# Performance work log

Measured on AMD Instinct MI355X. Metric: run time of the kernel, lower is better.

Reference implementation:

```python
import jax, jax.numpy as jnp
import numpy as np

B, N, D, R, STEPS = 16, 512, 512, 8, 2


def setup_inputs() -> dict:
    key = jax.random.key(0)
    ks = jax.random.split(key, 8)
    nodes = jax.random.normal(ks[0], (B, N, D), dtype=jnp.float32)
    edges = jax.random.uniform(ks[1], (B, R, N, N), dtype=jnp.float32)
    scale = 1.0 / np.sqrt(D)
    # per-relation Linear layers: weight [out,in] torch-style, bias [out]
    msg_W = jax.random.uniform(ks[2], (R, D, D), minval=-scale, maxval=scale, dtype=jnp.float32)
    msg_b = jax.random.uniform(ks[3], (R, D), minval=-scale, maxval=scale, dtype=jnp.float32)
    # GRUCell params, gate order (r, z, n) like torch
    w_ih = jax.random.uniform(ks[4], (3 * D, D), minval=-scale, maxval=scale, dtype=jnp.float32)
    w_hh = jax.random.uniform(ks[5], (3 * D, D), minval=-scale, maxval=scale, dtype=jnp.float32)
    b_ih = jax.random.uniform(ks[6], (3 * D,), minval=-scale, maxval=scale, dtype=jnp.float32)
    b_hh = jax.random.uniform(ks[7], (3 * D,), minval=-scale, maxval=scale, dtype=jnp.float32)
    return {"nodes": nodes, "edges": edges, "msg_W": msg_W, "msg_b": msg_b,
            "w_ih": w_ih, "w_hh": w_hh, "b_ih": b_ih, "b_hh": b_hh}


def reference(nodes, edges, msg_W, msg_b, w_ih, w_hh, b_ih, b_hh):
    # nodes: [b,n,d], edges: [b,R,n,n]
    h = nodes  # keep [b,n,d]; torch flattens to [b*n,d] but math is identical
    bias_sum = msg_b.sum(axis=0)  # sum of per-relation biases, [d]
    for _ in range(STEPS):
        # per-relation message passing: m[b,r,i,d] = edges[b,r] @ h[b]
        m = jnp.einsum('brij,bjd->brid', edges, h)
        # per-relation Linear (y = x @ W_r^T + b_r), summed over relations
        agg = jnp.einsum('brid,red->bie', m, msg_W) + bias_sum  # [b,n,d]
        # GRUCell update (gate order r, z, n)
        gi = agg @ w_ih.T + b_ih  # [b,n,3d]
        gh = h @ w_hh.T + b_hh    # [b,n,3d]
        ir, iz, i_n = jnp.split(gi, 3, axis=-1)
        hr, hz, h_n = jnp.split(gh, 3, axis=-1)
        r = jax.nn.sigmoid(ir + hr)
        z = jax.nn.sigmoid(iz + hz)
        n_t = jnp.tanh(i_n + r * h_n)
        h = (1.0 - z) * n_t + z * h
    return h.mean(axis=1)  # [b,d]
```

## Files before the change

kernel.cpp:

```cpp
#include <hip/hip_runtime.h>

typedef _Float16 f16;
typedef __attribute__((ext_vector_type(8))) _Float16 half8;
typedef __attribute__((ext_vector_type(4))) float f32x4;

struct f16x4 { f16 a, b, c, d; };


__global__ void cvt_fr(const float* __restrict__ in, f16* __restrict__ hi,
                       f16* __restrict__ lo, int n_units) {
  const int u = blockIdx.x * blockDim.x + threadIdx.x;
  if (u >= n_units) return;
  const int l = u & 63, kc = (u >> 6) & 15, rt = u >> 10;
  const long ibase = (long)(rt * 16 + (l & 15)) * 512 + kc * 32 + ((l >> 4) << 3);
  const float4 v0 = *(const float4*)(in + ibase);
  const float4 v1 = *(const float4*)(in + ibase + 4);
  const float v[8] = {v0.x, v0.y, v0.z, v0.w, v1.x, v1.y, v1.z, v1.w};
  half8 h, lw;
#pragma unroll
  for (int e = 0; e < 8; ++e) {
    h[e] = (f16)v[e];
    lw[e] = (f16)(v[e] - (float)h[e]);
  }
  *(half8*)(hi + (long)u * 8) = h;
  *(half8*)(lo + (long)u * 8) = lw;
}

__global__ void cvt_fr1(const float* __restrict__ in, f16* __restrict__ hi,
                        int n_units) {
  const int u = blockIdx.x * blockDim.x + threadIdx.x;
  if (u >= n_units) return;
  const int l = u & 63, kc = (u >> 6) & 15, rt = u >> 10;
  const long ibase = (long)(rt * 16 + (l & 15)) * 512 + kc * 32 + ((l >> 4) << 3);
  const float4 v0 = *(const float4*)(in + ibase);
  const float4 v1 = *(const float4*)(in + ibase + 4);
  const float v[8] = {v0.x, v0.y, v0.z, v0.w, v1.x, v1.y, v1.z, v1.w};
  half8 h;
#pragma unroll
  for (int e = 0; e < 8; ++e) h[e] = (f16)v[e];
  *(half8*)(hi + (long)u * 8) = h;
}

__global__ void bias_sum_k(const float* __restrict__ msg_b, float* __restrict__ bs) {
  int e = threadIdx.x;
  float s = 0.f;
  for (int r = 0; r < 8; ++r) s += msg_b[r * 512 + e];
  bs[e] = s;
}

template <int SA, int SB, int OUT, int SWZ>
__global__ __launch_bounds__(256, 2) void gemm_dr(
    const f16* __restrict__ Ah, const f16* __restrict__ Al,
    const f16* __restrict__ Bh, const f16* __restrict__ Bl,
    f16* __restrict__ Chi, f16* __restrict__ Clo, float* __restrict__ Cf,
    const float* __restrict__ bias, int N, int R, long sAr, long sBr,
    int zdiv, long sAzr, long sAzb, long sBzr, long sBzb,
    long sCzr, long sCzb) {
  __shared__ __align__(16) f16 smem[16384];
  const int tid = threadIdx.x;
  int bx, by, z;
  if constexpr (SWZ) {
    const int l = blockIdx.x;
    const int xcd = l & 7, m2 = l >> 3, zq = m2 >> 4, t = m2 & 15;
    z = (zq << 3) | xcd; bx = t & 3; by = t >> 2;
  } else {
    bx = blockIdx.x; by = blockIdx.y; z = blockIdx.z;
  }
  const int zr = z % zdiv, zb = z / zdiv;
  const int lane = tid & 63;
  const int w = tid >> 6;
  const int wm = (w & 1) << 6;
  const int wn = (w >> 1) << 6;

  const f16* pAh = Ah + (long)zr * sAzr + (long)zb * sAzb +
                   (long)(by * 8 + (wm >> 4)) * 8192 + lane * 8;
  const f16* pBh = Bh + (long)zr * sBzr + (long)zb * sBzb +
                   (long)(bx * 8 + (wn >> 4)) * 8192 + lane * 8;
  const f16* pAl = SA ? (Al + (pAh - Ah)) : nullptr;
  const f16* pBl = SB ? (Bl + (pBh - Bh)) : nullptr;
  const long cbase = (long)zr * sCzr + (long)zb * sCzb;

  f32x4 acc[4][4];
#pragma unroll
  for (int i = 0; i < 4; ++i)
#pragma unroll
    for (int j = 0; j < 4; ++j) acc[i][j] = (f32x4){0.f, 0.f, 0.f, 0.f};

  half8 fAh[2][4], fAl[2][4], fBh[2][4], fBl[2][4];
  const int NIT = R * 16;

  auto LD = [&](int bf, int ii) {
    const int r_ = ii >> 4, kc_ = ii & 15;
    const long oa = (long)r_ * sAr + kc_ * 512;
    const long ob = (long)r_ * sBr + kc_ * 512;
#pragma unroll
    for (int t = 0; t < 4; ++t) {
      fAh[bf][t] = *(const half8*)(pAh + t * 8192 + oa);
      if constexpr (SA) fAl[bf][t] = *(const half8*)(pAl + t * 8192 + oa);
      fBh[bf][t] = *(const half8*)(pBh + t * 8192 + ob);
      if constexpr (SB) fBl[bf][t] = *(const half8*)(pBl + t * 8192 + ob);
    }
  };
  auto MM = [&](int bf) {
#pragma unroll
    for (int mt = 0; mt < 4; ++mt)
#pragma unroll
      for (int nt = 0; nt < 4; ++nt) {
        acc[mt][nt] = __builtin_amdgcn_mfma_f32_16x16x32_f16(
            fAh[bf][mt], fBh[bf][nt], acc[mt][nt], 0, 0, 0);
        if constexpr (SB)
          acc[mt][nt] = __builtin_amdgcn_mfma_f32_16x16x32_f16(
              fAh[bf][mt], fBl[bf][nt], acc[mt][nt], 0, 0, 0);
        if constexpr (SA)
          acc[mt][nt] = __builtin_amdgcn_mfma_f32_16x16x32_f16(
              fAl[bf][mt], fBh[bf][nt], acc[mt][nt], 0, 0, 0);
      }
  };

  LD(0, 0);
  for (int i = 0; i < NIT; i += 2) {
    if (i + 1 < NIT) LD(1, i + 1);
    MM(0);
    if (i + 2 < NIT) LD(0, i + 2);
    if (i + 1 < NIT) MM(1);
  }

  const int l15 = lane & 15;
  const int rb = (lane >> 4) << 2;
  if constexpr (OUT) {
#pragma unroll
    for (int nt = 0; nt < 4; ++nt) {
      const int col = wn + nt * 16 + l15;
#pragma unroll
      for (int mt = 0; mt < 4; ++mt)
#pragma unroll
        for (int v = 0; v < 4; ++v) {
          const int row = wm + mt * 16 + rb + v;
          const float cval = acc[mt][nt][v];
          const f16 h = (f16)cval;
          smem[row * 128 + ((col >> 3) ^ (row & 15)) * 8 + (col & 7)] = h;
          acc[mt][nt][v] = cval - (float)h;
        }
    }
    __syncthreads();
#pragma unroll
    for (int i2 = 0; i2 < 8; ++i2) {
      const int u = i2 * 256 + tid;
      const int ul = u & 63, kc_loc = (u >> 6) & 3, rt_loc = u >> 8;
      const int row = rt_loc * 16 + (ul & 15);
      const int gcol = kc_loc * 4 + (ul >> 4);
      const int4 vv = *(const int4*)&smem[row * 128 + ((gcol ^ (row & 15)) << 3)];
      *(int4*)&Chi[cbase + ((long)(by * 8 + rt_loc) * 16 + bx * 4 + kc_loc) * 512 + ul * 8] = vv;
    }
    __syncthreads();
#pragma unroll
    for (int nt = 0; nt < 4; ++nt) {
      const int col = wn + nt * 16 + l15;
#pragma unroll
      for (int mt = 0; mt < 4; ++mt)
#pragma unroll
        for (int v = 0; v < 4; ++v) {
          const int row = wm + mt * 16 + rb + v;
          smem[row * 128 + ((col >> 3) ^ (row & 15)) * 8 + (col & 7)] = (f16)acc[mt][nt][v];
        }
    }
    __syncthreads();
#pragma unroll
    for (int i2 = 0; i2 < 8; ++i2) {
      const int u = i2 * 256 + tid;
      const int ul = u & 63, kc_loc = (u >> 6) & 3, rt_loc = u >> 8;
      const int row = rt_loc * 16 + (ul & 15);
      const int gcol = kc_loc * 4 + (ul >> 4);
      const int4 vv = *(const int4*)&smem[row * 128 + ((gcol ^ (row & 15)) << 3)];
      *(int4*)&Clo[cbase + ((long)(by * 8 + rt_loc) * 16 + bx * 4 + kc_loc) * 512 + ul * 8] = vv;
    }
  } else {
#pragma unroll
    for (int nt = 0; nt < 4; ++nt) {
      const int col = bx * 128 + wn + nt * 16 + l15;
      const float bv = bias ? bias[col] : 0.f;
#pragma unroll
      for (int mt = 0; mt < 4; ++mt) {
        const long rowbase = (long)(by * 128 + wm + mt * 16 + rb) * N + col;
#pragma unroll
        for (int v = 0; v < 4; ++v)
          Cf[cbase + rowbase + (long)v * N] = acc[mt][nt][v] + bv;
      }
    }
  }
}

__global__ void reduce_agg4(const f16* __restrict__ Phi, const f16* __restrict__ Plo,
                            const float* __restrict__ bsum,
                            f16* __restrict__ hi, f16* __restrict__ lo) {
  const long i = ((long)blockIdx.x * blockDim.x + threadIdx.x) * 4;
  const int li = (int)i;
  const int l = (li >> 3) & 63, kc = (li >> 9) & 15;
  const int e0 = kc * 32 + ((l >> 4) << 3) + (li & 4);
  const float4 b = *(const float4*)(bsum + e0);
  float v0 = b.x, v1 = b.y, v2 = b.z, v3 = b.w;
#pragma unroll
  for (int q = 0; q < 4; ++q) {
    const long o = (long)q * 4194304 + i;
    const f16x4 ph = *(const f16x4*)(Phi + o);
    const f16x4 pl = *(const f16x4*)(Plo + o);
    v0 += (float)ph.a + (float)pl.a;
    v1 += (float)ph.b + (float)pl.b;
    v2 += (float)ph.c + (float)pl.c;
    v3 += (float)ph.d + (float)pl.d;
  }
  f16x4 h, lw;
  h.a = (f16)v0; lw.a = (f16)(v0 - (float)h.a);
  h.b = (f16)v1; lw.b = (f16)(v1 - (float)h.b);
  h.c = (f16)v2; lw.c = (f16)(v2 - (float)h.c);
  h.d = (f16)v3; lw.d = (f16)(v3 - (float)h.d);
  *(f16x4*)(hi + i) = h;
  *(f16x4*)(lo + i) = lw;
}

__global__ void gru_k(const float* __restrict__ gi, const float* __restrict__ gh,
                      const float* __restrict__ holdf, f16* __restrict__ hhi) {
  const int u = blockIdx.x * blockDim.x + threadIdx.x;
  const int row = u >> 6, d0 = (u & 63) << 3;
  const long gbase = (long)row * 1536 + d0;
  const float4 giR0 = *(const float4*)(gi + gbase),      giR1 = *(const float4*)(gi + gbase + 4);
  const float4 giZ0 = *(const float4*)(gi + gbase + 512), giZ1 = *(const float4*)(gi + gbase + 516);
  const float4 giN0 = *(const float4*)(gi + gbase + 1024), giN1 = *(const float4*)(gi + gbase + 1028);
  const float4 ghR0 = *(const float4*)(gh + gbase),      ghR1 = *(const float4*)(gh + gbase + 4);
  const float4 ghZ0 = *(const float4*)(gh + gbase + 512), ghZ1 = *(const float4*)(gh + gbase + 516);
  const float4 ghN0 = *(const float4*)(gh + gbase + 1024), ghN1 = *(const float4*)(gh + gbase + 1028);
  const float irv[8] = {giR0.x, giR0.y, giR0.z, giR0.w, giR1.x, giR1.y, giR1.z, giR1.w};
  const float izv[8] = {giZ0.x, giZ0.y, giZ0.z, giZ0.w, giZ1.x, giZ1.y, giZ1.z, giZ1.w};
  const float inv[8] = {giN0.x, giN0.y, giN0.z, giN0.w, giN1.x, giN1.y, giN1.z, giN1.w};
  const float hrv[8] = {ghR0.x, ghR0.y, ghR0.z, ghR0.w, ghR1.x, ghR1.y, ghR1.z, ghR1.w};
  const float hzv[8] = {ghZ0.x, ghZ0.y, ghZ0.z, ghZ0.w, ghZ1.x, ghZ1.y, ghZ1.z, ghZ1.w};
  const float hnv[8] = {ghN0.x, ghN0.y, ghN0.z, ghN0.w, ghN1.x, ghN1.y, ghN1.z, ghN1.w};
  const long hflat = (long)(row >> 4) * 8192 + (d0 >> 5) * 512 +
                     ((row & 15) + (((d0 >> 3) & 3) << 4)) * 8;
  half8 hh8;
  if (!holdf) hh8 = *(const half8*)(hhi + hflat);
  half8 oh;
#pragma unroll
  for (int e = 0; e < 8; ++e) {
    const float h = holdf ? holdf[(long)row * 512 + d0 + e] : (float)hh8[e];
    const float r = 1.f / (1.f + __expf(-(irv[e] + hrv[e])));
    const float zg = 1.f / (1.f + __expf(-(izv[e] + hzv[e])));
    const float nt = tanhf(inv[e] + r * hnv[e]);
    const float o = (1.f - zg) * nt + zg * h;
    oh[e] = (f16)o;
  }
  *(half8*)(hhi + hflat) = oh;
}

__global__ void mean_k(const f16* __restrict__ hhi, float* __restrict__ out) {
  const int b = blockIdx.x;
  const int d = threadIdx.x;
  const long base = (long)b * 262144 + (d >> 5) * 512 + (((d >> 3) & 3) << 4) * 8 + (d & 7);
  float s = 0.f;
  for (int n = 0; n < 512; ++n) {
    const long j = base + (long)(n >> 4) * 8192 + (n & 15) * 8;
    s += (float)hhi[j];
  }
  out[b * 512 + d] = s * (1.f / 512.f);
}

extern "C" void kernel_launch(void* const* d_in, const int* in_sizes, int n_in,
                              void* d_out, int out_size, void* d_ws, size_t ws_size,
                              hipStream_t stream) {
  const float* nodes = (const float*)d_in[0];
  const float* edges = (const float*)d_in[1];
  const float* msg_W = (const float*)d_in[2];
  const float* msg_b = (const float*)d_in[3];
  const float* w_ih  = (const float*)d_in[4];
  const float* w_hh  = (const float*)d_in[5];
  const float* b_ih  = (const float*)d_in[6];
  const float* b_hh  = (const float*)d_in[7];
  float* out = (float*)d_out;

  char* ws = (char*)d_ws;
  size_t off = 0;
  auto alloc = [&](size_t bytes) -> char* {
    char* p = ws + off;
    off += (bytes + 1023) & ~(size_t)1023;
    return p;
  };
  f16* edges_hi = (f16*)alloc(33554432ull * 2);
  f16* W_hi     = (f16*)alloc(2097152ull * 2);
  f16* W_lo     = (f16*)alloc(2097152ull * 2);
  f16* wih_hi   = (f16*)alloc(786432ull * 2);
  f16* whh_hi   = (f16*)alloc(786432ull * 2);
  f16* h_hi     = (f16*)alloc(4194304ull * 2);
  f16* hWT_hi   = (f16*)alloc(33554432ull * 2);
  f16* hWT_lo   = (f16*)alloc(33554432ull * 2);
  f16* Phi      = (f16*)alloc(16777216ull * 2);
  f16* Plo      = (f16*)alloc(16777216ull * 2);
  float* bsum   = (float*)alloc(512 * 4);
  float* gi = (float*)hWT_hi;
  float* gh = (float*)hWT_lo;
  f16* agg_hi = hWT_hi + 25165824;
  f16* agg_lo = agg_hi + 4194304;

  cvt_fr1<<<16384, 256, 0, stream>>>(edges, edges_hi, 4194304);
  cvt_fr<<<1024,  256, 0, stream>>>(msg_W, W_hi, W_lo, 262144);
  cvt_fr1<<<384,  256, 0, stream>>>(w_ih, wih_hi, 98304);
  cvt_fr1<<<384,  256, 0, stream>>>(w_hh, whh_hi, 98304);
  cvt_fr1<<<2048, 256, 0, stream>>>(nodes, h_hi, 524288);
  bias_sum_k<<<1, 512, 0, stream>>>(msg_b, bsum);

  for (int step = 0; step < 2; ++step) {
    gemm_dr<1, 0, 1, 0><<<dim3(4, 4, 128), 256, 0, stream>>>(
        W_hi, W_lo, h_hi, nullptr, hWT_hi, hWT_lo, nullptr, nullptr,
        512, 1, 0L, 0L, 8, 262144L, 0L, 0L, 262144L, 262144L, 2097152L);
    gemm_dr<0, 1, 1, 1><<<dim3(1024, 1, 1), 256, 0, stream>>>(
        edges_hi, nullptr, hWT_hi, hWT_lo, Phi, Plo, nullptr, nullptr,
        512, 2, 262144L, 262144L, 4, 524288L, 2097152L, 524288L, 2097152L,
        4194304L, 262144L);
    reduce_agg4<<<4096, 256, 0, stream>>>(Phi, Plo, bsum, agg_hi, agg_lo);
    gemm_dr<1, 0, 0, 0><<<dim3(12, 64, 1), 256, 0, stream>>>(
        agg_hi, agg_lo, wih_hi, nullptr, nullptr, nullptr, gi, b_ih,
        1536, 1, 0L, 0L, 1, 0L, 0L, 0L, 0L, 0L, 0L);
    gemm_dr<0, 0, 0, 0><<<dim3(12, 64, 1), 256, 0, stream>>>(
        h_hi, nullptr, whh_hi, nullptr, nullptr, nullptr, gh, b_hh,
        1536, 1, 0L, 0L, 1, 0L, 0L, 0L, 0L, 0L, 0L);
    gru_k<<<2048, 256, 0, stream>>>(gi, gh, step ? nullptr : nodes, h_hi);
  }
  mean_k<<<16, 512, 0, stream>>>(h_hi, out);
}
```

Before: 817.6 us.

## Stage GEMM operand tiles through LDS with global_load_lds double buffering

```diff
diff --git a/kernel.cpp b/kernel.cpp
--- a/kernel.cpp
+++ b/kernel.cpp
@@ -6,6 +6,12 @@
 
 struct f16x4 { f16 a, b, c, d; };
 
+
+__device__ __forceinline__ void stage16(const f16* g, f16* l) {
+  __builtin_amdgcn_global_load_lds(
+      (const __attribute__((address_space(1))) void*)g,
+      (__attribute__((address_space(3))) void*)l, 16, 0, 0);
+}
 
 __global__ void cvt_fr(const float* __restrict__ in, f16* __restrict__ hi,
                        f16* __restrict__ lo, int n_units) {
@@ -49,14 +55,19 @@
 }
 
 template <int SA, int SB, int OUT, int SWZ>
-__global__ __launch_bounds__(256, 2) void gemm_dr(
+__global__ __launch_bounds__(256, 3) void gemm_dr(
     const f16* __restrict__ Ah, const f16* __restrict__ Al,
     const f16* __restrict__ Bh, const f16* __restrict__ Bl,
     f16* __restrict__ Chi, f16* __restrict__ Clo, float* __restrict__ Cf,
     const float* __restrict__ bias, int N, int R, long sAr, long sBr,
     int zdiv, long sAzr, long sAzb, long sBzr, long sBzb,
     long sCzr, long sCzb) {
-  __shared__ __align__(16) f16 smem[16384];
+  constexpr int NU = 8 * ((1 + SA) + (1 + SB));
+  constexpr int NW = NU / 4;
+  constexpr int BUF = NU * 512;
+  constexpr int SMEMN = (2 * BUF > 16384) ? 2 * BUF : 16384;
+  __shared__ __align__(16) f16 smem[SMEMN];
+
   const int tid = threadIdx.x;
   int bx, by, z;
   if constexpr (SWZ) {
@@ -72,12 +83,10 @@
   const int wm = (w & 1) << 6;
   const int wn = (w >> 1) << 6;
 
-  const f16* pAh = Ah + (long)zr * sAzr + (long)zb * sAzb +
-                   (long)(by * 8 + (wm >> 4)) * 8192 + lane * 8;
-  const f16* pBh = Bh + (long)zr * sBzr + (long)zb * sBzb +
-                   (long)(bx * 8 + (wn >> 4)) * 8192 + lane * 8;
-  const f16* pAl = SA ? (Al + (pAh - Ah)) : nullptr;
-  const f16* pBl = SB ? (Bl + (pBh - Bh)) : nullptr;
+  const f16* gA = Ah + (long)zr * sAzr + (long)zb * sAzb + (long)by * 65536 + lane * 8;
+  const f16* gB = Bh + (long)zr * sBzr + (long)zb * sBzb + (long)bx * 65536 + lane * 8;
+  const f16* gAl = SA ? (Al + (gA - Ah)) : nullptr;
+  const f16* gBl = SB ? (Bl + (gB - Bh)) : nullptr;
   const long cbase = (long)zr * sCzr + (long)zb * sCzb;
 
   f32x4 acc[4][4];
@@ -86,44 +95,68 @@
 #pragma unroll
     for (int j = 0; j < 4; ++j) acc[i][j] = (f32x4){0.f, 0.f, 0.f, 0.f};
 
-  half8 fAh[2][4], fAl[2][4], fBh[2][4], fBl[2][4];
   const int NIT = R * 16;
 
-  auto LD = [&](int bf, int ii) {
-    const int r_ = ii >> 4, kc_ = ii & 15;
-    const long oa = (long)r_ * sAr + kc_ * 512;
-    const long ob = (long)r_ * sBr + kc_ * 512;
-#pragma unroll
-    for (int t = 0; t < 4; ++t) {
-      fAh[bf][t] = *(const half8*)(pAh + t * 8192 + oa);
-      if constexpr (SA) fAl[bf][t] = *(const half8*)(pAl + t * 8192 + oa);
-      fBh[bf][t] = *(const half8*)(pBh + t * 8192 + ob);
-      if constexpr (SB) fBl[bf][t] = *(const half8*)(pBl + t * 8192 + ob);
+  auto ST = [&](int bf, int ii) {
+    const long oa = (long)(ii >> 4) * sAr + (ii & 15) * 512;
+    const long ob = (long)(ii >> 4) * sBr + (ii & 15) * 512;
+    f16* lb = &smem[bf * BUF];
+#pragma unroll
+    for (int q = 0; q < NW; ++q) {
+      const int s = w * NW + q;
+      const f16* src;
+      if (s < 8) {
+        src = gA + (long)s * 8192 + oa;
+      } else if (SA && s < 16) {
+        src = gAl + (long)(s - 8) * 8192 + oa;
+      } else {
+        const int sb = s - 8 * (1 + SA);
+        src = (SB && sb >= 8) ? (gBl + (long)(sb - 8) * 8192 + ob)
+                              : (gB + (long)sb * 8192 + ob);
+      }
+      stage16(src, lb + s * 512);
     }
   };
-  auto MM = [&](int bf) {
-#pragma unroll
-    for (int mt = 0; mt < 4; ++mt)
+
+  auto CP = [&](int bf) {
+    const f16* lb = &smem[bf * BUF];
+    const int lo8 = lane * 8;
+    half8 bh[4], bl[4];
+#pragma unroll
+    for (int nt = 0; nt < 4; ++nt) {
+      const int ub = 8 * (1 + SA) + (w >> 1) * 4 + nt;
+      bh[nt] = *(const half8*)(lb + ub * 512 + lo8);
+      if constexpr (SB) bl[nt] = *(const half8*)(lb + (ub + 8) * 512 + lo8);
+    }
+#pragma unroll
+    for (int mt = 0; mt < 4; ++mt) {
+      const int ua = (w & 1) * 4 + mt;
+      const half8 ah = *(const half8*)(lb + ua * 512 + lo8);
+      half8 al;
+      if constexpr (SA) al = *(const half8*)(lb + (ua + 8) * 512 + lo8);
 #pragma unroll
       for (int nt = 0; nt < 4; ++nt) {
         acc[mt][nt] = __builtin_amdgcn_mfma_f32_16x16x32_f16(
-            fAh[bf][mt], fBh[bf][nt], acc[mt][nt], 0, 0, 0);
+            ah, bh[nt], acc[mt][nt], 0, 0, 0);
         if constexpr (SB)
           acc[mt][nt] = __builtin_amdgcn_mfma_f32_16x16x32_f16(
-              fAh[bf][mt], fBl[bf][nt], acc[mt][nt], 0, 0, 0);
+              ah, bl[nt], acc[mt][nt], 0, 0, 0);
         if constexpr (SA)
           acc[mt][nt] = __builtin_amdgcn_mfma_f32_16x16x32_f16(
-              fAl[bf][mt], fBh[bf][nt], acc[mt][nt], 0, 0, 0);
+              al, bh[nt], acc[mt][nt], 0, 0, 0);
       }
+    }
   };
 
-  LD(0, 0);
-  for (int i = 0; i < NIT; i += 2) {
-    if (i + 1 < NIT) LD(1, i + 1);
-    MM(0);
-    if (i + 2 < NIT) LD(0, i + 2);
-    if (i + 1 < NIT) MM(1);
-  }
+  ST(0, 0);
+  int cur = 0;
+  for (int t = 0; t < NIT; ++t) {
+    __syncthreads();
+    if (t + 1 < NIT) ST(cur ^ 1, t + 1);
+    CP(cur);
+    cur ^= 1;
+  }
+  __syncthreads();
 
   const int l15 = lane & 15;
   const int rb = (lane >> 4) << 2;
```

Measured after the change: 770.3 us. 5.8% less time.
